# Optimization experiments

Hardware: AMD Instinct MI355X
Metric: run time of the kernel (lower is better)

Reference implementation:

```python
import jax, jax.numpy as jnp
import numpy as np

DIM = 4096
N_HEADS = 32
N_KV_HEADS = 8
HEAD_DIM = 128
ROPE_THETA = 10000.0
REPEATS = N_HEADS // N_KV_HEADS
SCALE = HEAD_DIM ** -0.5


def rope(x, seq_len, offset):
    # x: [b, h, seq_len, head_dim]; faithful to source: cos/sin from cat((freqs,freqs)),
    # rotate built by interleaved pair swap then flatten.
    d = x.shape[-1]
    inv_freq = 1.0 / (ROPE_THETA ** (jnp.arange(0, d, 2, dtype=jnp.float32) / d))  # [d/2]
    t = jnp.arange(offset, offset + seq_len, dtype=jnp.float32)                    # [L]
    freqs = t[:, None] * inv_freq[None, :]                                         # [L, d/2]
    emb = jnp.concatenate([freqs, freqs], axis=-1)                                 # [L, d]
    cos_emb = jnp.cos(emb)
    sin_emb = jnp.sin(emb)
    x_even = x[..., 0::2]
    x_odd = x[..., 1::2]
    rotate_x = jnp.stack([-x_odd, x_even], axis=-1).reshape(x.shape)
    return x * cos_emb + rotate_x * sin_emb


def setup_inputs() -> dict:
    key = jax.random.key(0)
    k1, k2, k3, k4, k5 = jax.random.split(key, 5)
    b, l = 1, 2048
    s = 0.02
    x = jax.random.normal(k1, (b, l, DIM), dtype=jnp.float32)
    wq = jax.random.normal(k2, (DIM, N_HEADS * HEAD_DIM), dtype=jnp.float32) * s
    wk = jax.random.normal(k3, (DIM, N_KV_HEADS * HEAD_DIM), dtype=jnp.float32) * s
    wv = jax.random.normal(k4, (DIM, N_KV_HEADS * HEAD_DIM), dtype=jnp.float32) * s
    wo = jax.random.normal(k5, (N_HEADS * HEAD_DIM, DIM), dtype=jnp.float32) * s
    return {"x": x, "wq": wq, "wk": wk, "wv": wv, "wo": wo, "seq_len": l}


def reference(x, wq, wk, wv, wo, seq_len):
    b, l, _ = x.shape
    q = (x @ wq).reshape(b, l, N_HEADS, HEAD_DIM).transpose(0, 2, 1, 3)       # [b,H,l,d]
    k = (x @ wk).reshape(b, l, N_KV_HEADS, HEAD_DIM).transpose(0, 2, 1, 3)    # [b,Hk,l,d]
    v = (x @ wv).reshape(b, l, N_KV_HEADS, HEAD_DIM).transpose(0, 2, 1, 3)
    # repeat KV heads to match query heads (GQA)
    k = jnp.repeat(k, REPEATS, axis=1)   # [b,H,l,d]
    v = jnp.repeat(v, REPEATS, axis=1)
    offset = 0  # cache is None
    q = rope(q, seq_len, offset)
    k = rope(k, seq_len, offset)
    scores = jnp.einsum('bhid,bhjd->bhij', q * SCALE, k)
    scores = jax.nn.softmax(scores.astype(jnp.float32), axis=-1).astype(scores.dtype)
    out = jnp.einsum('bhij,bhjd->bhid', scores, v)
    out = out.transpose(0, 2, 1, 3).reshape(b, l, N_HEADS * HEAD_DIM)
    return out @ wo, (k, v)
```

## Files before the change

kernel.cpp:

```cpp
#include <hip/hip_runtime.h>
#include <cstdint>
#include <cstddef>

#define DIM 4096
#define SEQ 2048
#define NH 32
#define NKV 8
#define HD 128
#define QKVN 6144

typedef __bf16 bf16_t;
typedef __bf16 bf16x8 __attribute__((ext_vector_type(8)));
typedef __bf16 bf16x4 __attribute__((ext_vector_type(4)));
typedef __bf16 bf16x2 __attribute__((ext_vector_type(2)));
typedef float f32x4 __attribute__((ext_vector_type(4)));
typedef int int4v __attribute__((ext_vector_type(4)));

__device__ __forceinline__ f32x4 mfma16(bf16x8 a, bf16x8 b, f32x4 c) {
  return __builtin_amdgcn_mfma_f32_16x16x32_bf16(a, b, c, 0, 0, 0);
}

__device__ __forceinline__ void async16(const bf16_t* g, bf16_t* l) {
  __builtin_amdgcn_global_load_lds((__attribute__((address_space(1))) void*)g,
                                   (__attribute__((address_space(3))) void*)l,
                                   16, 0, 0);
}

__device__ __forceinline__ int pack2(float a, float b) {
  bf16x2 h = { (bf16_t)a, (bf16_t)b };
  return __builtin_bit_cast(int, h);
}

#define LGKM0() do { asm volatile("s_waitcnt lgkmcnt(0)" ::: "memory"); \
                     __builtin_amdgcn_sched_barrier(0); } while (0)

template <int N> __device__ __forceinline__ void vmw() {
  if constexpr (N == 6) asm volatile("s_waitcnt vmcnt(6)" ::: "memory");
  else if constexpr (N == 7) asm volatile("s_waitcnt vmcnt(7)" ::: "memory");
  __builtin_amdgcn_sched_barrier(0);
}

__global__ void cast_x(const float* __restrict__ x, bf16_t* __restrict__ xb) {
  int i = blockIdx.x * 256 + threadIdx.x;
  const float4 v = ((const float4*)x)[i];
  bf16x4 o = { (bf16_t)v.x, (bf16_t)v.y, (bf16_t)v.z, (bf16_t)v.w };
  *(bf16x4*)(xb + (size_t)i * 4) = o;
}

__global__ void tcast(const float* __restrict__ src, bf16_t* __restrict__ dst,
                      int Ncols, int Kdim) {
  __shared__ float tile[32][33];
  int n0 = blockIdx.x * 32, k0 = blockIdx.y * 32;
  int tx = threadIdx.x, ty = threadIdx.y;
#pragma unroll
  for (int r = 0; r < 4; r++)
    tile[ty + 8 * r][tx] = src[(size_t)(k0 + ty + 8 * r) * Ncols + n0 + tx];
  __syncthreads();
#pragma unroll
  for (int r = 0; r < 4; r++)
    dst[(size_t)(n0 + ty + 8 * r) * Kdim + k0 + tx] = (bf16_t)tile[tx][ty + 8 * r];
}

template <int NF>
__global__ __launch_bounds__(512) void gemm256(const bf16_t* __restrict__ A,
                                               const bf16_t* __restrict__ Bt,
                                               float* __restrict__ C,
                                               int M, int N, int K) {
  constexpr int NLOAD = 4 + NF;
  __shared__ bf16_t As[2][16384];
  __shared__ bf16_t Bs[2][NF * 4096];
  const int t = threadIdx.x;
  const int lane = t & 63;
  const int l15 = lane & 15, quad = lane >> 4;
  const int w = t >> 6, wm = w >> 2, wn = w & 3;
  const int cgx = l15 & 7;

  const int gx = gridDim.x;
  const int nwg = gx * gridDim.y;
  const int id = blockIdx.y * gx + blockIdx.x;
  const int swz = (id & 7) * (nwg >> 3) + (id >> 3);
  const int bm = (swz / gx) * 256, bn = (swz % gx) * (NF * 64);

  const int srow = t >> 3;
  const int scol = ((t & 7) ^ (srow & 7)) << 3;
  const bf16_t* gA = A + (size_t)(bm + srow) * K + scol;
  const bf16_t* gB = Bt + (size_t)(bn + srow) * K + scol;
  const int ldst = t * 8;

  f32x4 acc[8][NF] = {};

  auto stageT = [&](int b2, int kk) {
    async16(gA + kk, &As[b2][ldst]);
    async16(gA + (size_t)64 * K + kk, &As[b2][4096 + ldst]);
    async16(gA + (size_t)128 * K + kk, &As[b2][8192 + ldst]);
    async16(gA + (size_t)192 * K + kk, &As[b2][12288 + ldst]);
    async16(gB + kk, &Bs[b2][ldst]);
    async16(gB + (size_t)64 * K + kk, &Bs[b2][4096 + ldst]);
    if constexpr (NF == 3) async16(gB + (size_t)128 * K + kk, &Bs[b2][8192 + ldst]);
  };

  stageT(0, 0);
  stageT(1, 64);
  vmw<NLOAD>();
  __builtin_amdgcn_s_barrier();

  auto tile = [&](int b2, int knext) {
    bf16x8 afl[4][2], afh[4][2], bf01[2][2], bf2[2];
#pragma unroll
    for (int mi = 0; mi < 4; mi++)
#pragma unroll
      for (int s = 0; s < 2; s++)
        afl[mi][s] = *(const bf16x8*)&As[b2][(wm * 64 + mi * 16 + l15) * 64 +
                                            ((((s << 2) | quad) ^ cgx) << 3)];
#pragma unroll
    for (int ni = 0; ni < 2; ni++)
#pragma unroll
      for (int s = 0; s < 2; s++)
        bf01[ni][s] = *(const bf16x8*)&Bs[b2][(ni * 64 + wn * 16 + l15) * 64 +
                                              ((((s << 2) | quad) ^ cgx) << 3)];
    __builtin_amdgcn_s_barrier();
    LGKM0();
    __builtin_amdgcn_s_setprio(1);
#pragma unroll
    for (int mi = 0; mi < 4; mi++)
#pragma unroll
      for (int ni = 0; ni < 2; ni++)
#pragma unroll
        for (int s = 0; s < 2; s++)
          acc[mi][ni] = mfma16(afl[mi][s], bf01[ni][s], acc[mi][ni]);
    __builtin_amdgcn_s_setprio(0);
    __builtin_amdgcn_s_barrier();

#pragma unroll
    for (int mi = 0; mi < 4; mi++)
#pragma unroll
      for (int s = 0; s < 2; s++)
        afh[mi][s] = *(const bf16x8*)&As[b2][(128 + wm * 64 + mi * 16 + l15) * 64 +
                                             ((((s << 2) | quad) ^ cgx) << 3)];
    if constexpr (NF == 2) {
      LGKM0();
      __builtin_amdgcn_s_barrier();
      stageT(b2, knext);
      __builtin_amdgcn_sched_barrier(0);
    } else {
      __builtin_amdgcn_s_barrier();
      LGKM0();
    }
    __builtin_amdgcn_s_setprio(1);
#pragma unroll
    for (int mi = 0; mi < 4; mi++)
#pragma unroll
      for (int ni = 0; ni < 2; ni++)
#pragma unroll
        for (int s = 0; s < 2; s++)
          acc[mi + 4][ni] = mfma16(afh[mi][s], bf01[ni][s], acc[mi + 4][ni]);
    __builtin_amdgcn_s_setprio(0);
    if constexpr (NF == 2) vmw<NLOAD>();
    __builtin_amdgcn_s_barrier();

    if constexpr (NF == 3) {
#pragma unroll
      for (int s = 0; s < 2; s++)
        bf2[s] = *(const bf16x8*)&Bs[b2][(128 + wn * 16 + l15) * 64 +
                                         ((((s << 2) | quad) ^ cgx) << 3)];
      LGKM0();
      __builtin_amdgcn_s_barrier();
      stageT(b2, knext);
      __builtin_amdgcn_sched_barrier(0);
      __builtin_amdgcn_s_setprio(1);
#pragma unroll
      for (int mi = 0; mi < 4; mi++)
#pragma unroll
        for (int s = 0; s < 2; s++) {
          acc[mi][2] = mfma16(afl[mi][s], bf2[s], acc[mi][2]);
          acc[mi + 4][2] = mfma16(afh[mi][s], bf2[s], acc[mi + 4][2]);
        }
      __builtin_amdgcn_s_setprio(0);
      vmw<NLOAD>();
      __builtin_amdgcn_s_barrier();
    }
  };

  const int nit = K >> 7;
  for (int i = 0; i < nit; ++i) {
    tile(0, ((i << 7) + 128) & (K - 1));
    tile(1, ((i << 7) + 192) & (K - 1));
  }

#pragma unroll
  for (int mi = 0; mi < 8; mi++)
#pragma unroll
    for (int ni = 0; ni < NF; ni++) {
      size_t row = (size_t)bm + (mi >> 2) * 128 + wm * 64 + (mi & 3) * 16 + quad * 4;
      size_t col = (size_t)bn + ni * 64 + wn * 16 + l15;
#pragma unroll
      for (int r = 0; r < 4; r++)
        C[(row + r) * N + col] = acc[mi][ni][r];
    }
}

__global__ void rope_scatter(const float* __restrict__ qkv, bf16_t* __restrict__ Qb,
                             bf16_t* __restrict__ Kb, bf16_t* __restrict__ Vt,
                             float* __restrict__ kOut, float* __restrict__ vOut) {
  int idx = blockIdx.x * 256 + threadIdx.x;
  int t = idx / 3072;
  int p = idx - t * 3072;
  const float NEG_L2T_64 = -0.20762050593046f;
  const float SS = 0.08838834764831845f * 1.4426950408889634f;
  if (p < 2048) {
    int hh = p >> 6, pr = p & 63;
    int d0 = pr << 1;
    const float* src = qkv + (size_t)t * QKVN + hh * HD + d0;
    float a = src[0], b = src[1];
    int j0 = d0 & 63, j1 = (d0 + 1) & 63;
    float th0 = (float)t * exp2f((float)j0 * NEG_L2T_64);
    float th1 = (float)t * exp2f((float)j1 * NEG_L2T_64);
    float o0 = (a * cosf(th0) - b * sinf(th0)) * SS;
    float o1 = (b * cosf(th1) + a * sinf(th1)) * SS;
    bf16_t* dst = Qb + ((size_t)hh * SEQ + t) * HD + d0;
    dst[0] = (bf16_t)o0;
    dst[1] = (bf16_t)o1;
  } else if (p < 2560) {
    int q2 = p - 2048;
    int kh = q2 >> 6, pr = q2 & 63;
    int d0 = pr << 1;
    const float* src = qkv + (size_t)t * QKVN + 4096 + kh * HD + d0;
    float a = src[0], b = src[1];
    int j0 = d0 & 63, j1 = (d0 + 1) & 63;
    float th0 = (float)t * exp2f((float)j0 * NEG_L2T_64);
    float th1 = (float)t * exp2f((float)j1 * NEG_L2T_64);
    float o0 = a * cosf(th0) - b * sinf(th0);
    float o1 = b * cosf(th1) + a * sinf(th1);
    bf16_t* dst = Kb + ((size_t)kh * SEQ + t) * HD + d0;
    dst[0] = (bf16_t)o0;
    dst[1] = (bf16_t)o1;
#pragma unroll
    for (int rep = 0; rep < 4; rep++) {
      float* kp = kOut + ((size_t)(kh * 4 + rep) * SEQ + t) * HD + d0;
      kp[0] = o0;
      kp[1] = o1;
    }
  } else {
    int q2 = p - 2560;
    int kh = q2 >> 6, pr = q2 & 63;
    int d0 = pr << 1;
    const float* src = qkv + (size_t)t * QKVN + 5120 + kh * HD + d0;
    float a = src[0], b = src[1];
#pragma unroll
    for (int rep = 0; rep < 4; rep++) {
      float* vp = vOut + ((size_t)(kh * 4 + rep) * SEQ + t) * HD + d0;
      vp[0] = a;
      vp[1] = b;
    }
    int tp = (t & ~31) + ((t & 12) << 1) + (t & 3) + ((t & 16) >> 2);
    Vt[((size_t)kh * HD + d0) * SEQ + tp] = (bf16_t)a;
    Vt[((size_t)kh * HD + d0 + 1) * SEQ + tp] = (bf16_t)b;
  }
}

__global__ __launch_bounds__(512, 2) void attn_kernel(const bf16_t* __restrict__ Qb,
                                                      const bf16_t* __restrict__ Kb,
                                                      const bf16_t* __restrict__ Vt,
                                                      bf16_t* __restrict__ AO) {
  __shared__ bf16_t Ks[2][8192];
  __shared__ bf16_t Vs[2][8192];
  const int h = blockIdx.y, kh = h >> 2;
  const int qbase = blockIdx.x * 256;
  const int w = threadIdx.x >> 6, lane = threadIdx.x & 63;
  const int l15 = lane & 15, quad = lane >> 4;
  const bf16_t* KbH = Kb + (size_t)kh * SEQ * HD;
  const bf16_t* VtH = Vt + (size_t)kh * HD * SEQ;

  bf16x8 qf[2][4];
#pragma unroll
  for (int nq = 0; nq < 2; nq++) {
    const bf16_t* qp = Qb + ((size_t)h * SEQ + qbase + w * 32 + nq * 16 + l15) * HD + quad * 8;
#pragma unroll
    for (int kc = 0; kc < 4; kc++) qf[nq][kc] = *(const bf16x8*)(qp + kc * 32);
  }

  f32x4 acc[8][2] = {};
  float rsum[2] = {0.f, 0.f};

  auto stage = [&](int buf, int kt0) {
    if (w < 4) {
      int kc = w;
#pragma unroll
      for (int kg = 0; kg < 4; kg++) {
        const bf16_t* g = KbH + (size_t)(kt0 + kg * 16 + (lane >> 2)) * HD + kc * 32 + (lane & 3) * 8;
        async16(g, &Ks[buf][kc * 2048 + kg * 512]);
      }
    } else {
      int vi = w - 4, kt = vi >> 1, dg0 = (vi & 1) * 4;
#pragma unroll
      for (int j = 0; j < 4; j++) {
        int dg = dg0 + j;
        const bf16_t* g = VtH + (size_t)(dg * 16 + (lane >> 2)) * SEQ + kt0 + kt * 32 + (lane & 3) * 8;
        async16(g, &Vs[buf][kt * 4096 + dg * 512]);
      }
    }
  };

  stage(0, 0);
  int buf = 0;

  for (int kt0 = 0; kt0 < SEQ; kt0 += 64, buf ^= 1) {
    __syncthreads();
    if (kt0 + 64 < SEQ) stage(buf ^ 1, kt0 + 64);

    f32x4 sacc[4][2] = {};
#pragma unroll
    for (int mi = 0; mi < 4; mi++)
#pragma unroll
      for (int kc = 0; kc < 4; kc++) {
        bf16x8 kf = *(const bf16x8*)(&Ks[buf][(kc * 64 + mi * 16 + l15) * 32 + quad * 8]);
#pragma unroll
        for (int nq = 0; nq < 2; nq++)
          sacc[mi][nq] = mfma16(kf, qf[nq][kc], sacc[mi][nq]);
      }

    int pk[4][2][2];
#pragma unroll
    for (int mi = 0; mi < 4; mi++)
#pragma unroll
      for (int nq = 0; nq < 2; nq++) {
        float p0 = exp2f(sacc[mi][nq][0]);
        float p1 = exp2f(sacc[mi][nq][1]);
        float p2 = exp2f(sacc[mi][nq][2]);
        float p3 = exp2f(sacc[mi][nq][3]);
        rsum[nq] += (p0 + p1) + (p2 + p3);
        pk[mi][nq][0] = pack2(p0, p1);
        pk[mi][nq][1] = pack2(p2, p3);
      }

#pragma unroll
    for (int kt = 0; kt < 2; kt++) {
#pragma unroll
      for (int nq = 0; nq < 2; nq++) {
        int4v dw;
        dw[0] = pk[2 * kt][nq][0];
        dw[1] = pk[2 * kt][nq][1];
        dw[2] = pk[2 * kt + 1][nq][0];
        dw[3] = pk[2 * kt + 1][nq][1];
        bf16x8 pf = __builtin_bit_cast(bf16x8, dw);
#pragma unroll
        for (int dt = 0; dt < 8; dt++) {
          bf16x8 vf = *(const bf16x8*)(&Vs[buf][(kt * 128 + dt * 16 + l15) * 32 + quad * 8]);
          acc[dt][nq] = mfma16(vf, pf, acc[dt][nq]);
        }
      }
    }
  }

#pragma unroll
  for (int nq = 0; nq < 2; nq++) {
    float rs = rsum[nq];
    rs += __shfl_xor(rs, 16);
    rs += __shfl_xor(rs, 32);
    float inv = 1.0f / rs;
    int q = qbase + w * 32 + nq * 16 + l15;
#pragma unroll
    for (int dt = 0; dt < 8; dt++) {
      bf16x4 o = { (bf16_t)(acc[dt][nq][0] * inv), (bf16_t)(acc[dt][nq][1] * inv),
                   (bf16_t)(acc[dt][nq][2] * inv), (bf16_t)(acc[dt][nq][3] * inv) };
      *(bf16x4*)(AO + (size_t)q * DIM + h * HD + dt * 16 + quad * 4) = o;
    }
  }
}

extern "C" void kernel_launch(void* const* d_in, const int* in_sizes, int n_in,
                              void* d_out, int out_size, void* d_ws, size_t ws_size,
                              hipStream_t stream) {
  const float* x = (const float*)d_in[0];
  const float* wq = (const float*)d_in[1];
  const float* wk = (const float*)d_in[2];
  const float* wv = (const float*)d_in[3];
  const float* wo = (const float*)d_in[4];
  float* out = (float*)d_out;
  float* kOut = out + (size_t)SEQ * DIM;
  float* vOut = kOut + (size_t)NH * SEQ * HD;

  char* ws = (char*)d_ws;
  bf16_t* Xb = (bf16_t*)ws;
  bf16_t* WT = (bf16_t*)(ws + 16777216);
  float* QKV = (float*)(ws + 67108864);
  bf16_t* WoT = (bf16_t*)(ws + 67108864);
  bf16_t* Qb = (bf16_t*)(ws + 117440512);
  bf16_t* Kb = (bf16_t*)(ws + 134217728);
  bf16_t* Vt = (bf16_t*)(ws + 138412032);
  bf16_t* AO = Xb;

  dim3 tb(32, 8);
  cast_x<<<8192, 256, 0, stream>>>(x, Xb);
  tcast<<<dim3(128, 128), tb, 0, stream>>>(wq, WT, 4096, 4096);
  tcast<<<dim3(32, 128), tb, 0, stream>>>(wk, WT + (size_t)4096 * 4096, 1024, 4096);
  tcast<<<dim3(32, 128), tb, 0, stream>>>(wv, WT + (size_t)5120 * 4096, 1024, 4096);
  gemm256<3><<<dim3(32, 8), 512, 0, stream>>>(Xb, WT, QKV, 2048, 6144, 4096);
  rope_scatter<<<24576, 256, 0, stream>>>(QKV, Qb, Kb, Vt, kOut, vOut);
  tcast<<<dim3(128, 128), tb, 0, stream>>>(wo, WoT, 4096, 4096);
  attn_kernel<<<dim3(8, 32), 512, 0, stream>>>(Qb, Kb, Vt, AO);
  gemm256<2><<<dim3(32, 8), 512, 0, stream>>>(AO, WoT, out, 2048, 4096, 4096);
}
```

Measured before the change: 537.8 us.

## Split GEMM tile prefetch into phased loads interleaved with MFMA stages

Restructures the GEMM K-loop from loading a whole tile into the current buffer after it is consumed to issuing next-tile loads in pieces into the other buffer, spread across the MFMA phases. The wait counts are retuned so each phase only waits for the part it needs. The goal is to overlap global-to-LDS transfers with compute and shorten the stalls at the end of each tile. In exchange there is only one tile of prefetch distance, and the hand-set vmcnt values must match the load order exactly or the kernel can read stale LDS.

```diff
diff --git a/kernel.cpp b/kernel.cpp
--- a/kernel.cpp
+++ b/kernel.cpp
@@ -35,8 +35,9 @@
                      __builtin_amdgcn_sched_barrier(0); } while (0)
 
 template <int N> __device__ __forceinline__ void vmw() {
-  if constexpr (N == 6) asm volatile("s_waitcnt vmcnt(6)" ::: "memory");
-  else if constexpr (N == 7) asm volatile("s_waitcnt vmcnt(7)" ::: "memory");
+  if constexpr (N == 2) asm volatile("s_waitcnt vmcnt(2)" ::: "memory");
+  else if constexpr (N == 3) asm volatile("s_waitcnt vmcnt(3)" ::: "memory");
+  else if constexpr (N == 4) asm volatile("s_waitcnt vmcnt(4)" ::: "memory");
   __builtin_amdgcn_sched_barrier(0);
 }
 
@@ -66,7 +67,6 @@
                                                const bf16_t* __restrict__ Bt,
                                                float* __restrict__ C,
                                                int M, int N, int K) {
-  constexpr int NLOAD = 4 + NF;
   __shared__ bf16_t As[2][16384];
   __shared__ bf16_t Bs[2][NF * 4096];
   const int t = threadIdx.x;
@@ -89,23 +89,42 @@
 
   f32x4 acc[8][NF] = {};
 
-  auto stageT = [&](int b2, int kk) {
+  auto stP0 = [&](int b2, int kk) {
     async16(gA + kk, &As[b2][ldst]);
     async16(gA + (size_t)64 * K + kk, &As[b2][4096 + ldst]);
+    if constexpr (NF == 2) {
+      async16(gB + kk, &Bs[b2][ldst]);
+      async16(gB + (size_t)64 * K + kk, &Bs[b2][4096 + ldst]);
+    }
+  };
+  auto stP1 = [&](int b2, int kk) {
+    if constexpr (NF == 3) {
+      async16(gB + kk, &Bs[b2][ldst]);
+      async16(gB + (size_t)64 * K + kk, &Bs[b2][4096 + ldst]);
+    } else {
+      async16(gA + (size_t)128 * K + kk, &As[b2][8192 + ldst]);
+      async16(gA + (size_t)192 * K + kk, &As[b2][12288 + ldst]);
+    }
+  };
+  auto stP2 = [&](int b2, int kk) {
     async16(gA + (size_t)128 * K + kk, &As[b2][8192 + ldst]);
     async16(gA + (size_t)192 * K + kk, &As[b2][12288 + ldst]);
-    async16(gB + kk, &Bs[b2][ldst]);
-    async16(gB + (size_t)64 * K + kk, &Bs[b2][4096 + ldst]);
-    if constexpr (NF == 3) async16(gB + (size_t)128 * K + kk, &Bs[b2][8192 + ldst]);
+    async16(gB + (size_t)128 * K + kk, &Bs[b2][8192 + ldst]);
   };
 
-  stageT(0, 0);
-  stageT(1, 64);
-  vmw<NLOAD>();
+  stP0(0, 0);
+  stP1(0, 0);
+  if constexpr (NF == 3) stP2(0, 0);
+  if constexpr (NF == 3) vmw<3>(); else vmw<2>();
   __builtin_amdgcn_s_barrier();
 
-  auto tile = [&](int b2, int knext) {
+  const int nkt = K >> 6;
+  for (int kt = 0; kt < nkt; ++kt) {
+    const int b2 = kt & 1, bo = b2 ^ 1;
+    const int kn = (kt + 1 == nkt) ? 0 : (kt + 1) << 6;
+
     bf16x8 afl[4][2], afh[4][2], bf01[2][2], bf2[2];
+
 #pragma unroll
     for (int mi = 0; mi < 4; mi++)
 #pragma unroll
@@ -118,6 +137,7 @@
       for (int s = 0; s < 2; s++)
         bf01[ni][s] = *(const bf16x8*)&Bs[b2][(ni * 64 + wn * 16 + l15) * 64 +
                                               ((((s << 2) | quad) ^ cgx) << 3)];
+    stP0(bo, kn);
     __builtin_amdgcn_s_barrier();
     LGKM0();
     __builtin_amdgcn_s_setprio(1);
@@ -129,6 +149,7 @@
         for (int s = 0; s < 2; s++)
           acc[mi][ni] = mfma16(afl[mi][s], bf01[ni][s], acc[mi][ni]);
     __builtin_amdgcn_s_setprio(0);
+    if constexpr (NF == 3) vmw<3>(); else vmw<4>();
     __builtin_amdgcn_s_barrier();
 
 #pragma unroll
@@ -137,15 +158,9 @@
       for (int s = 0; s < 2; s++)
         afh[mi][s] = *(const bf16x8*)&As[b2][(128 + wm * 64 + mi * 16 + l15) * 64 +
                                              ((((s << 2) | quad) ^ cgx) << 3)];
-    if constexpr (NF == 2) {
-      LGKM0();
-      __builtin_amdgcn_s_barrier();
-      stageT(b2, knext);
-      __builtin_amdgcn_sched_barrier(0);
-    } else {
-      __builtin_amdgcn_s_barrier();
-      LGKM0();
-    }
+    stP1(bo, kn);
+    __builtin_amdgcn_s_barrier();
+    LGKM0();
     __builtin_amdgcn_s_setprio(1);
 #pragma unroll
     for (int mi = 0; mi < 4; mi++)
@@ -155,7 +170,7 @@
         for (int s = 0; s < 2; s++)
           acc[mi + 4][ni] = mfma16(afh[mi][s], bf01[ni][s], acc[mi + 4][ni]);
     __builtin_amdgcn_s_setprio(0);
-    if constexpr (NF == 2) vmw<NLOAD>();
+    if constexpr (NF == 3) vmw<4>(); else vmw<2>();
     __builtin_amdgcn_s_barrier();
 
     if constexpr (NF == 3) {
@@ -163,10 +178,9 @@
       for (int s = 0; s < 2; s++)
         bf2[s] = *(const bf16x8*)&Bs[b2][(128 + wn * 16 + l15) * 64 +
                                          ((((s << 2) | quad) ^ cgx) << 3)];
+      stP2(bo, kn);
+      __builtin_amdgcn_s_barrier();
       LGKM0();
-      __builtin_amdgcn_s_barrier();
-      stageT(b2, knext);
-      __builtin_amdgcn_sched_barrier(0);
       __builtin_amdgcn_s_setprio(1);
 #pragma unroll
       for (int mi = 0; mi < 4; mi++)
@@ -176,15 +190,9 @@
           acc[mi + 4][2] = mfma16(afh[mi][s], bf2[s], acc[mi + 4][2]);
         }
       __builtin_amdgcn_s_setprio(0);
-      vmw<NLOAD>();
+      vmw<3>();
       __builtin_amdgcn_s_barrier();
     }
-  };
-
-  const int nit = K >> 7;
-  for (int i = 0; i < nit; ++i) {
-    tile(0, ((i << 7) + 128) & (K - 1));
-    tile(1, ((i << 7) + 192) & (K - 1));
   }
 
 #pragma unroll
@@ -197,6 +205,7 @@
       for (int r = 0; r < 4; r++)
         C[(row + r) * N + col] = acc[mi][ni][r];
     }
+  asm volatile("s_waitcnt vmcnt(0)" ::: "memory");
 }
 
 __global__ void rope_scatter(const float* __restrict__ qkv, bf16_t* __restrict__ Qb,
```

After: 522.5 us. -2.8%, faster.
